# Performance work log

Hardware: AMD Instinct MI355X
Metric: run time of the kernel (lower is better)

The kernel has to match this reference:

```python
import jax, jax.numpy as jnp
from jax import lax
import numpy as np

NODE_COUNT = 4096
BATCH = 128
THRESHOLD = 1.0
DISSIPATION = 0.1
SPARSITY = 0.9
MAX_ITERS = 100


def setup_inputs() -> dict:
    key = jax.random.key(0)
    k_in, k_conn, k_mask, k_w, k_b = jax.random.split(key, 5)
    input_data = jax.random.normal(k_in, (BATCH, NODE_COUNT), dtype=jnp.float32)
    conn = jax.random.normal(k_conn, (NODE_COUNT, NODE_COUNT), dtype=jnp.float32)
    mask = (jax.random.uniform(k_mask, (NODE_COUNT, NODE_COUNT)) > SPARSITY).astype(jnp.float32)
    conn = conn * mask
    conn = conn / (jnp.abs(conn).sum(axis=1, keepdims=True) + 1e-6)
    # input_proj: Linear(node_count, node_count), torch default init scale
    bound = 1.0 / np.sqrt(NODE_COUNT)
    W = jax.random.uniform(k_w, (NODE_COUNT, NODE_COUNT), minval=-bound, maxval=bound, dtype=jnp.float32)
    b = jax.random.uniform(k_b, (NODE_COUNT,), minval=-bound, maxval=bound, dtype=jnp.float32)
    return {"input_data": input_data, "W": W, "b": b, "connections": conn}


def _avalanche(state, connections):
    """Batched avalanche scan with per-sample sticky early-exit (torch break)."""
    B = state.shape[0]
    done0 = jnp.zeros((B,), dtype=bool)
    total0 = jnp.zeros((B,), dtype=state.dtype)

    def step(carry, _):
        state, done, total = carry
        active = (state > THRESHOLD).astype(state.dtype)          # [B, N]
        n_active = active.sum(axis=1)                              # [B]
        new_done = done | (n_active == 0)                          # break condition
        total = total + jnp.where(new_done, 0.0, n_active)
        # propagated = connections @ active  (per sample)
        prop = jnp.einsum('ij,bj->bi', connections, active)        # [B, N]
        new_state = (state * (1.0 - DISSIPATION) + prop * (1.0 - active)) * (1.0 - active)
        state = jnp.where(new_done[:, None], state, new_state)
        return (state, new_done, total), None

    (state, done, total), _ = lax.scan(step, (state, done0, total0), None, length=MAX_ITERS)
    return state, total


def reference(input_data, W, b, connections):
    projected = input_data @ W.T + b                               # [B, N]
    output, sizes = _avalanche(projected, connections)
    max_size = sizes.max()
    return output, max_size
```

## Files before the change

### kernel.cpp

```cpp
#include <hip/hip_runtime.h>

#define N_NODES 4096
#define BATCH 128
#define SPLITK 8
#define GBN 32
#define GBK 64
#define KCHUNK (N_NODES / SPLITK)
#define NSTEP (KCHUNK / GBK)
#define GEMM_BLOCKS ((N_NODES / GBN) * SPLITK)
#define TRANS_BLOCKS 1024

typedef _Float16 f16x4 __attribute__((ext_vector_type(4)));
typedef _Float16 f16x8 __attribute__((ext_vector_type(8)));
typedef float f32x4 __attribute__((ext_vector_type(4)));
typedef unsigned int u32x4 __attribute__((ext_vector_type(4)));

__device__ __forceinline__ void dma16(const void* g, void* l) {
#if defined(__has_builtin) && __has_builtin(__builtin_amdgcn_global_load_lds)
  __builtin_amdgcn_global_load_lds((const __attribute__((address_space(1))) void*)g,
                                   (__attribute__((address_space(3))) void*)l, 16, 0, 0);
#else
  *(u32x4*)l = *(const u32x4*)g;
#endif
}

#if defined(__has_builtin)
#if __has_builtin(__builtin_amdgcn_cvt_f32_fp8) && __has_builtin(__builtin_amdgcn_cvt_pk_fp8_f32)
#define CONN_FP8 1
#endif
#endif
#ifndef CONN_FP8
#define CONN_FP8 0
#endif

#if CONN_FP8
#define CONN_ELEM_BYTES 1
#define CONN_SCALE (1.0f / 256.0f)
#else
#define CONN_ELEM_BYTES 2
#define CONN_SCALE 1.0f
#endif

__device__ __forceinline__ void conn_store4(void* out, size_t off, float4 v) {
#if CONN_FP8
  unsigned int p = __builtin_amdgcn_cvt_pk_fp8_f32(v.x * 256.0f, v.y * 256.0f, 0, false);
  p = (unsigned int)__builtin_amdgcn_cvt_pk_fp8_f32(v.z * 256.0f, v.w * 256.0f, (int)p, true);
  *(unsigned int*)((unsigned char*)out + off) = p;
#else
  const unsigned int ux = __float_as_uint(v.x), uy = __float_as_uint(v.y);
  const unsigned int uz = __float_as_uint(v.z), uw = __float_as_uint(v.w);
  ushort4 u;
  u.x = (unsigned short)((ux + 0x7FFFu + ((ux >> 16) & 1u)) >> 16);
  u.y = (unsigned short)((uy + 0x7FFFu + ((uy >> 16) & 1u)) >> 16);
  u.z = (unsigned short)((uz + 0x7FFFu + ((uz >> 16) & 1u)) >> 16);
  u.w = (unsigned short)((uw + 0x7FFFu + ((uw >> 16) & 1u)) >> 16);
  *(ushort4*)((unsigned short*)out + off) = u;
#endif
}

__device__ __forceinline__ float4 conn_load4(const void* cT, int j, int t) {
#if CONN_FP8
  const unsigned int c = *(const unsigned int*)((const unsigned char*)cT + ((size_t)j << 12) + t * 4);
  return make_float4(__builtin_amdgcn_cvt_f32_fp8(c, 0), __builtin_amdgcn_cvt_f32_fp8(c, 1),
                     __builtin_amdgcn_cvt_f32_fp8(c, 2), __builtin_amdgcn_cvt_f32_fp8(c, 3));
#else
  const ushort4 c = *(const ushort4*)((const unsigned short*)cT + ((size_t)j << 12) + t * 4);
  return make_float4(__uint_as_float((unsigned int)c.x << 16),
                     __uint_as_float((unsigned int)c.y << 16),
                     __uint_as_float((unsigned int)c.z << 16),
                     __uint_as_float((unsigned int)c.w << 16));
#endif
}

__global__ __launch_bounds__(256) void asplit_kernel(const float* __restrict__ in,
                                                     _Float16* __restrict__ Ah,
                                                     _Float16* __restrict__ Al,
                                                     unsigned int* __restrict__ maxslot) {
  if (blockIdx.x == 0 && threadIdx.x == 0) *maxslot = 0u;
  const size_t idx = ((size_t)blockIdx.x * 256 + threadIdx.x) * 4;
  const float4 v = *(const float4*)(in + idx);
  f16x4 hi, lo;
  const float x0 = v.x * 256.f, x1 = v.y * 256.f, x2 = v.z * 256.f, x3 = v.w * 256.f;
  hi[0] = (_Float16)x0; lo[0] = (_Float16)(x0 - (float)hi[0]);
  hi[1] = (_Float16)x1; lo[1] = (_Float16)(x1 - (float)hi[1]);
  hi[2] = (_Float16)x2; lo[2] = (_Float16)(x2 - (float)hi[2]);
  hi[3] = (_Float16)x3; lo[3] = (_Float16)(x3 - (float)hi[3]);
  *(f16x4*)(Ah + idx) = hi;
  *(f16x4*)(Al + idx) = lo;
}

struct GemmSmem {
  alignas(16) _Float16 Ah[2][128 * GBK];
  alignas(16) _Float16 Al[2][128 * GBK];
  alignas(16) float B[2][GBN * GBK];
};
struct TransSmem { float tile[4][64][65]; };
union PrepSmem { GemmSmem g; TransSmem t; };

__global__ __launch_bounds__(256, 2) void fused_prep_kernel(
    const _Float16* __restrict__ Ahp, const _Float16* __restrict__ Alp,
    const float* __restrict__ W, const float* __restrict__ conn,
    float* __restrict__ P, void* __restrict__ connT) {
  __shared__ PrepSmem sm;
  const int tid = threadIdx.x;
  const int bid = blockIdx.x;
  const int wave = tid >> 6, lane = tid & 63;

  if (bid < GEMM_BLOCKS) {
    const int wm = wave >> 1, wn = wave & 1;
    const int g = lane >> 4, lrow = lane & 15;
    const int n0 = (bid & 127) * GBN;
    const int kb = (bid >> 7) * KCHUNK;

    const char* AsrcBase = (const char*)((wave >> 1) ? Alp : Ahp);
    const int ac0 = (wave & 1) * 8;
    const int arow_l = lane >> 3;
    const int ainrow = (((lane & 7) << 4) ^ ((lane >> 3) << 4));
    const int brow_l = lane >> 4;
    const int binrow0 = (lane & 15) << 4;

    auto issue = [&](int buf, int t) {
      const size_t kbyteA = (size_t)(kb + t * GBK) * 2;
      const size_t kbyteB = (size_t)(kb + t * GBK) * 4;
      char* AldsB = (char*)((wave >> 1) ? sm.g.Al[buf] : sm.g.Ah[buf]);
#pragma unroll
      for (int i = 0; i < 8; ++i) {
        const int c = ac0 + i;
        const int row = 8 * c + arow_l;
        dma16(AsrcBase + (size_t)row * (N_NODES * 2) + kbyteA + ainrow,
              AldsB + c * 1024 + lane * 16);
      }
#pragma unroll
      for (int i = 0; i < 2; ++i) {
        const int c = wave * 2 + i;
        const int row = 4 * c + brow_l;
        dma16((const char*)W + (size_t)(n0 + row) * (N_NODES * 4) + kbyteB +
                  (binrow0 ^ ((row & 7) << 4)),
              (char*)sm.g.B[buf] + c * 1024 + lane * 16);
      }
    };

    f32x4 acc[4] = {};
    issue(0, 0);
    issue(1, 1);

#pragma unroll
    for (int t = 0; t < NSTEP; ++t) {
      const int cur = t & 1;
      if (t + 1 < NSTEP) asm volatile("s_waitcnt vmcnt(10)" ::: "memory");
      else               asm volatile("s_waitcnt vmcnt(0)" ::: "memory");
      __builtin_amdgcn_sched_barrier(0);
      __builtin_amdgcn_s_barrier();
      __builtin_amdgcn_sched_barrier(0);

#pragma unroll
      for (int kk = 0; kk < 2; ++kk) {
        const int br = wn * 16 + lrow;
        const char* bbase = (const char*)sm.g.B[cur] + br * 256;
        const int bm = (br & 7) << 4;
        const int cb = (kk * 32 + g * 8) * 4;
        const f32x4 b0 = *(const f32x4*)(bbase + ((cb) ^ bm));
        const f32x4 b1 = *(const f32x4*)(bbase + ((cb + 16) ^ bm));
        f16x8 bh, bl;
#pragma unroll
        for (int j = 0; j < 4; ++j) {
          const float x = b0[j] * 64.f;
          const _Float16 h = (_Float16)x;
          bh[j] = h; bl[j] = (_Float16)(x - (float)h);
          const float y = b1[j] * 64.f;
          const _Float16 h2 = (_Float16)y;
          bh[4 + j] = h2; bl[4 + j] = (_Float16)(y - (float)h2);
        }
#pragma unroll
        for (int fm = 0; fm < 4; ++fm) {
          const int ar = wm * 64 + fm * 16 + lrow;
          const int am = (ar & 7) << 4;
          const int ca = (kk * 32 + g * 8) * 2;
          const f16x8 ah = *(const f16x8*)((const char*)sm.g.Ah[cur] + ar * 128 + (ca ^ am));
          const f16x8 al = *(const f16x8*)((const char*)sm.g.Al[cur] + ar * 128 + (ca ^ am));
          acc[fm] = __builtin_amdgcn_mfma_f32_16x16x32_f16(ah, bh, acc[fm], 0, 0, 0);
          acc[fm] = __builtin_amdgcn_mfma_f32_16x16x32_f16(ah, bl, acc[fm], 0, 0, 0);
          acc[fm] = __builtin_amdgcn_mfma_f32_16x16x32_f16(al, bh, acc[fm], 0, 0, 0);
        }
      }

      __builtin_amdgcn_sched_barrier(0);
      __builtin_amdgcn_s_barrier();
      __builtin_amdgcn_sched_barrier(0);
      if (t + 2 < NSTEP) issue(cur, t + 2);
    }

    constexpr float INV = 1.0f / 16384.0f;
    float* Pb = P + (size_t)(bid >> 7) * BATCH * N_NODES;
    const int n = n0 + wn * 16 + lrow;
#pragma unroll
    for (int fm = 0; fm < 4; ++fm)
#pragma unroll
      for (int reg = 0; reg < 4; ++reg) {
        const int m = wm * 64 + fm * 16 + g * 4 + reg;
        Pb[(size_t)m * N_NODES + n] = acc[fm][reg] * INV;
      }
  } else {
    const int tile_id = (bid - GEMM_BLOCKS) * 4 + wave;
    const int bx = tile_id & 63, by = tile_id >> 6;
    float (*T)[65] = sm.t.tile[wave];
    const int lr = lane >> 4;
    const int lc = lane & 15;
#pragma unroll
    for (int i = 0; i < 16; ++i) {
      const int r = lr + 4 * i;
      const float4 v = *(const float4*)(conn + (size_t)(by * 64 + r) * N_NODES + bx * 64 + lc * 4);
      T[r][lc * 4 + 0] = v.x; T[r][lc * 4 + 1] = v.y;
      T[r][lc * 4 + 2] = v.z; T[r][lc * 4 + 3] = v.w;
    }
#pragma unroll
    for (int i = 0; i < 16; ++i) {
      const int orow = lr + 4 * i;
      float4 v;
      v.x = T[lc * 4 + 0][orow];
      v.y = T[lc * 4 + 1][orow];
      v.z = T[lc * 4 + 2][orow];
      v.w = T[lc * 4 + 3][orow];
      conn_store4(connT, (size_t)(bx * 64 + orow) * N_NODES + by * 64 + lc * 4, v);
    }
  }
}

__global__ __launch_bounds__(256) void proj_gemm_valu(const float* __restrict__ A,
                                                      const float* __restrict__ W,
                                                      float* __restrict__ P,
                                                      unsigned int* __restrict__ maxslot) {
  if (blockIdx.x == 0 && threadIdx.x == 0) *maxslot = 0u;
  __shared__ float As[16][132];
  __shared__ float Bs[16][68];
  const int tid = threadIdx.x;
  const int n0 = blockIdx.x * 64;
  const int tx = tid & 15, ty = tid >> 4;
  const int arow = tid >> 1, acol = (tid & 1) * 8;
  const int brow = tid >> 2, bcol = (tid & 3) * 4;
  float acc[2][4][4] = {};
  const float* Aptr = A + (size_t)arow * N_NODES + acol;
  const float* Wptr = W + (size_t)(n0 + brow) * N_NODES + bcol;
  for (int k0 = 0; k0 < N_NODES; k0 += 16) {
    const float4 a0 = *(const float4*)(Aptr + k0);
    const float4 a1 = *(const float4*)(Aptr + k0 + 4);
    const float4 bv = *(const float4*)(Wptr + k0);
    __syncthreads();
    As[acol + 0][arow] = a0.x; As[acol + 1][arow] = a0.y;
    As[acol + 2][arow] = a0.z; As[acol + 3][arow] = a0.w;
    As[acol + 4][arow] = a1.x; As[acol + 5][arow] = a1.y;
    As[acol + 6][arow] = a1.z; As[acol + 7][arow] = a1.w;
    Bs[bcol + 0][brow] = bv.x; Bs[bcol + 1][brow] = bv.y;
    Bs[bcol + 2][brow] = bv.z; Bs[bcol + 3][brow] = bv.w;
    __syncthreads();
#pragma unroll
    for (int kk = 0; kk < 16; ++kk) {
      const float4 av0 = *(const float4*)&As[kk][ty * 4];
      const float4 av1 = *(const float4*)&As[kk][64 + ty * 4];
      const float4 bv4 = *(const float4*)&Bs[kk][tx * 4];
      const float am[8] = {av0.x, av0.y, av0.z, av0.w, av1.x, av1.y, av1.z, av1.w};
      const float bn[4] = {bv4.x, bv4.y, bv4.z, bv4.w};
#pragma unroll
      for (int i2 = 0; i2 < 2; ++i2)
#pragma unroll
        for (int i = 0; i < 4; ++i)
#pragma unroll
          for (int j = 0; j < 4; ++j)
            acc[i2][i][j] += am[i2 * 4 + i] * bn[j];
    }
  }
#pragma unroll
  for (int i2 = 0; i2 < 2; ++i2)
#pragma unroll
    for (int i = 0; i < 4; ++i) {
      const int m = i2 * 64 + ty * 4 + i;
      *(float4*)(P + (size_t)m * N_NODES + n0 + tx * 4) =
          make_float4(acc[i2][i][0], acc[i2][i][1], acc[i2][i][2], acc[i2][i][3]);
    }
}

__global__ __launch_bounds__(256) void bias_inplace_kernel(float* __restrict__ P,
                                                           const float* __restrict__ bias) {
  const size_t base = ((size_t)blockIdx.x * 256 + threadIdx.x) * 4;
  const int n = (int)(base & (N_NODES - 1));
  float4 s = *(const float4*)(P + base);
  const float4 bv = *(const float4*)(bias + n);
  s.x += bv.x; s.y += bv.y; s.z += bv.z; s.w += bv.w;
  *(float4*)(P + base) = s;
}

template <int MODE, int NSPLIT>
__global__ __launch_bounds__(1024) void avalanche_kernel(const float* __restrict__ Pin,
                                                         const float* __restrict__ bias,
                                                         const void* __restrict__ connv,
                                                         float* __restrict__ out,
                                                         unsigned int* __restrict__ maxslot) {
  const int b = blockIdx.x;
  const int t = threadIdx.x;
  __shared__ unsigned long long mask[64];
  __shared__ int wincl[64];
  __shared__ int list[N_NODES];

  float4 s;
  if (MODE == 1) {
    const float4 bv = *(const float4*)(bias + t * 4);
    s = bv;
#pragma unroll
    for (int sp = 0; sp < NSPLIT; ++sp) {
      const float4 v = *(const float4*)(Pin + (size_t)sp * BATCH * N_NODES +
                                        (size_t)b * N_NODES + t * 4);
      s.x += v.x; s.y += v.y; s.z += v.z; s.w += v.w;
    }
  } else {
    s = *(const float4*)(Pin + (size_t)b * N_NODES + t * 4);
  }

  float total = 0.0f;

  for (int it = 0; it < 100; ++it) {
    const float v0 = s.x, v1 = s.y, v2 = s.z, v3 = s.w;
    unsigned int bits = 0;
    if (v0 > 1.0f) bits |= 1u;
    if (v1 > 1.0f) bits |= 2u;
    if (v2 > 1.0f) bits |= 4u;
    if (v3 > 1.0f) bits |= 8u;

    __syncthreads();
    if (t < 64) mask[t] = 0ULL;
    __syncthreads();
    if (bits) atomicOr(&mask[t >> 4], (unsigned long long)bits << ((t & 15) * 4));
    __syncthreads();

    if (t < 64) {
      int incl = __popcll(mask[t]);
#pragma unroll
      for (int d = 1; d < 64; d <<= 1) {
        const int y = __shfl_up(incl, d);
        if (t >= d) incl += y;
      }
      wincl[t] = incl;
    }
    __syncthreads();
    const int n = wincl[63];
    if (n == 0) break;
    total += (float)n;

    if (t < 64) {
      unsigned long long m = mask[t];
      int o = wincl[t] - __popcll(m);
      while (m) {
        list[o++] = (t << 6) + __builtin_ctzll(m);
        m &= m - 1;
      }
    }
    __syncthreads();

    float4 a0 = make_float4(0.f, 0.f, 0.f, 0.f), a1 = a0, a2 = a0, a3 = a0;
    if (MODE == 1) {
      int idx = 0;
      for (; idx + 8 <= n; idx += 8) {
        const float4 c0 = conn_load4(connv, list[idx + 0], t);
        const float4 c1 = conn_load4(connv, list[idx + 1], t);
        const float4 c2 = conn_load4(connv, list[idx + 2], t);
        const float4 c3 = conn_load4(connv, list[idx + 3], t);
        const float4 c4 = conn_load4(connv, list[idx + 4], t);
        const float4 c5 = conn_load4(connv, list[idx + 5], t);
        const float4 c6 = conn_load4(connv, list[idx + 6], t);
        const float4 c7 = conn_load4(connv, list[idx + 7], t);
        a0.x += c0.x; a0.y += c0.y; a0.z += c0.z; a0.w += c0.w;
        a1.x += c1.x; a1.y += c1.y; a1.z += c1.z; a1.w += c1.w;
        a2.x += c2.x; a2.y += c2.y; a2.z += c2.z; a2.w += c2.w;
        a3.x += c3.x; a3.y += c3.y; a3.z += c3.z; a3.w += c3.w;
        a0.x += c4.x; a0.y += c4.y; a0.z += c4.z; a0.w += c4.w;
        a1.x += c5.x; a1.y += c5.y; a1.z += c5.z; a1.w += c5.w;
        a2.x += c6.x; a2.y += c6.y; a2.z += c6.z; a2.w += c6.w;
        a3.x += c7.x; a3.y += c7.y; a3.z += c7.z; a3.w += c7.w;
      }
      for (; idx < n; ++idx) {
        const float4 c = conn_load4(connv, list[idx], t);
        a0.x += c.x; a0.y += c.y; a0.z += c.z; a0.w += c.w;
      }
    } else {
      const float* conn = (const float*)connv;
      for (int idx = 0; idx < n; ++idx) {
        const int j = list[idx];
        a0.x += conn[(size_t)(t * 4 + 0) * N_NODES + j];
        a0.y += conn[(size_t)(t * 4 + 1) * N_NODES + j];
        a0.z += conn[(size_t)(t * 4 + 2) * N_NODES + j];
        a0.w += conn[(size_t)(t * 4 + 3) * N_NODES + j];
      }
    }
    const float sc = (MODE == 1) ? CONN_SCALE : 1.0f;
    const float4 acc = make_float4(((a0.x + a1.x) + (a2.x + a3.x)) * sc,
                                   ((a0.y + a1.y) + (a2.y + a3.y)) * sc,
                                   ((a0.z + a1.z) + (a2.z + a3.z)) * sc,
                                   ((a0.w + a1.w) + (a2.w + a3.w)) * sc);

    s.x = (v0 > 1.0f) ? 0.0f : 0.9f * v0 + acc.x;
    s.y = (v1 > 1.0f) ? 0.0f : 0.9f * v1 + acc.y;
    s.z = (v2 > 1.0f) ? 0.0f : 0.9f * v2 + acc.z;
    s.w = (v3 > 1.0f) ? 0.0f : 0.9f * v3 + acc.w;
  }

  *(float4*)(out + (size_t)b * N_NODES + t * 4) = s;
  if (t == 0) atomicMax(maxslot, __float_as_uint(total));
}

extern "C" void kernel_launch(void* const* d_in, const int* in_sizes, int n_in,
                              void* d_out, int out_size, void* d_ws, size_t ws_size,
                              hipStream_t stream) {
  const float* input = (const float*)d_in[0];
  const float* W     = (const float*)d_in[1];
  const float* bias  = (const float*)d_in[2];
  const float* conn  = (const float*)d_in[3];
  float* out = (float*)d_out;

  const size_t aplane_bytes = (size_t)BATCH * N_NODES * 2;
  const size_t connT_bytes  = (size_t)N_NODES * N_NODES * CONN_ELEM_BYTES;
  const size_t part_bytes   = (size_t)SPLITK * BATCH * N_NODES * sizeof(float);
  unsigned int* maxslot = (unsigned int*)(out + (size_t)BATCH * N_NODES);

  if (ws_size >= 2 * aplane_bytes + connT_bytes + part_bytes) {
    _Float16* Ah = (_Float16*)d_ws;
    _Float16* Al = (_Float16*)((char*)d_ws + aplane_bytes);
    void* connT  = (char*)d_ws + 2 * aplane_bytes;
    float* part  = (float*)((char*)d_ws + 2 * aplane_bytes + connT_bytes);
    asplit_kernel<<<BATCH * N_NODES / 1024, 256, 0, stream>>>(input, Ah, Al, maxslot);
    fused_prep_kernel<<<GEMM_BLOCKS + TRANS_BLOCKS, 256, 0, stream>>>(Ah, Al, W, conn, part,
                                                                      connT);
    avalanche_kernel<1, SPLITK><<<BATCH, 1024, 0, stream>>>(part, bias, connT, out, maxslot);
  } else {
    proj_gemm_valu<<<dim3(N_NODES / 64, 1), 256, 0, stream>>>(input, W, out, maxslot);
    bias_inplace_kernel<<<BATCH * N_NODES / 1024, 256, 0, stream>>>(out, bias);
    avalanche_kernel<0, 1><<<BATCH, 1024, 0, stream>>>(out, nullptr, conn, out, maxslot);
  }
}
```

Measured before the change: 70.17 us.

## Enlarge GEMM tile to 128x128 with interleaved hi/lo A layout

Restructures the projection GEMM so each block computes a 128x128 output tile, up from 128x32. It reads W once per block and splits it into hi/lo halves once per fragment, then reuses those fragments across four M-fragments, which cuts redundant W traffic and conversion work. The input split now writes hi and lo halves interleaved into a single buffer, so one DMA stream feeds both. Split-K doubles to 16, which doubles the partial-sum buffer the avalanche kernel must reduce, and the 4x4 accumulator array raises register pressure.

```diff
diff --git a/kernel.cpp b/kernel.cpp
--- a/kernel.cpp
+++ b/kernel.cpp
@@ -2,9 +2,9 @@
 
 #define N_NODES 4096
 #define BATCH 128
-#define SPLITK 8
-#define GBN 32
-#define GBK 64
+#define SPLITK 16
+#define GBN 128
+#define GBK 32
 #define KCHUNK (N_NODES / SPLITK)
 #define NSTEP (KCHUNK / GBK)
 #define GEMM_BLOCKS ((N_NODES / GBN) * SPLITK)
@@ -73,11 +73,12 @@
 }
 
 __global__ __launch_bounds__(256) void asplit_kernel(const float* __restrict__ in,
-                                                     _Float16* __restrict__ Ah,
-                                                     _Float16* __restrict__ Al,
+                                                     _Float16* __restrict__ As,
                                                      unsigned int* __restrict__ maxslot) {
   if (blockIdx.x == 0 && threadIdx.x == 0) *maxslot = 0u;
   const size_t idx = ((size_t)blockIdx.x * 256 + threadIdx.x) * 4;
+  const int m = (int)(idx >> 12);
+  const int k = (int)(idx & (N_NODES - 1));
   const float4 v = *(const float4*)(in + idx);
   f16x4 hi, lo;
   const float x0 = v.x * 256.f, x1 = v.y * 256.f, x2 = v.z * 256.f, x3 = v.w * 256.f;
@@ -85,22 +86,21 @@
   hi[1] = (_Float16)x1; lo[1] = (_Float16)(x1 - (float)hi[1]);
   hi[2] = (_Float16)x2; lo[2] = (_Float16)(x2 - (float)hi[2]);
   hi[3] = (_Float16)x3; lo[3] = (_Float16)(x3 - (float)hi[3]);
-  *(f16x4*)(Ah + idx) = hi;
-  *(f16x4*)(Al + idx) = lo;
+  const size_t base = (size_t)m * 8192 + (size_t)(k >> 5) * 64 + (k & 31);
+  *(f16x4*)(As + base) = hi;
+  *(f16x4*)(As + base + 32) = lo;
 }
 
 struct GemmSmem {
-  alignas(16) _Float16 Ah[2][128 * GBK];
-  alignas(16) _Float16 Al[2][128 * GBK];
-  alignas(16) float B[2][GBN * GBK];
+  alignas(16) _Float16 A[2][128 * 64];
+  alignas(16) float B[2][128 * 32];
 };
 struct TransSmem { float tile[4][64][65]; };
 union PrepSmem { GemmSmem g; TransSmem t; };
 
 __global__ __launch_bounds__(256, 2) void fused_prep_kernel(
-    const _Float16* __restrict__ Ahp, const _Float16* __restrict__ Alp,
-    const float* __restrict__ W, const float* __restrict__ conn,
-    float* __restrict__ P, void* __restrict__ connT) {
+    const _Float16* __restrict__ As, const float* __restrict__ W,
+    const float* __restrict__ conn, float* __restrict__ P, void* __restrict__ connT) {
   __shared__ PrepSmem sm;
   const int tid = threadIdx.x;
   const int bid = blockIdx.x;
@@ -109,80 +109,78 @@
   if (bid < GEMM_BLOCKS) {
     const int wm = wave >> 1, wn = wave & 1;
     const int g = lane >> 4, lrow = lane & 15;
-    const int n0 = (bid & 127) * GBN;
-    const int kb = (bid >> 7) * KCHUNK;
-
-    const char* AsrcBase = (const char*)((wave >> 1) ? Alp : Ahp);
-    const int ac0 = (wave & 1) * 8;
-    const int arow_l = lane >> 3;
-    const int ainrow = (((lane & 7) << 4) ^ ((lane >> 3) << 4));
-    const int brow_l = lane >> 4;
-    const int binrow0 = (lane & 15) << 4;
+    const int n0 = (bid & 31) * GBN;
+    const int kb = (bid >> 5) * KCHUNK;
+    const int crow = lane >> 3;
+    const int q = lane & 7;
 
     auto issue = [&](int buf, int t) {
-      const size_t kbyteA = (size_t)(kb + t * GBK) * 2;
-      const size_t kbyteB = (size_t)(kb + t * GBK) * 4;
-      char* AldsB = (char*)((wave >> 1) ? sm.g.Al[buf] : sm.g.Ah[buf]);
-#pragma unroll
-      for (int i = 0; i < 8; ++i) {
-        const int c = ac0 + i;
-        const int row = 8 * c + arow_l;
-        dma16(AsrcBase + (size_t)row * (N_NODES * 2) + kbyteA + ainrow,
-              AldsB + c * 1024 + lane * 16);
-      }
-#pragma unroll
-      for (int i = 0; i < 2; ++i) {
-        const int c = wave * 2 + i;
-        const int row = 4 * c + brow_l;
-        dma16((const char*)W + (size_t)(n0 + row) * (N_NODES * 4) + kbyteB +
-                  (binrow0 ^ ((row & 7) << 4)),
+      const size_t abyte = (size_t)((kb >> 5) + t) * 128;
+      const size_t bbyte = (size_t)(kb + t * GBK) * 4;
+#pragma unroll
+      for (int i = 0; i < 4; ++i) {
+        const int c = wave * 4 + i;
+        const int row = c * 8 + crow;
+        dma16((const char*)As + (size_t)row * 16384 + abyte + ((q ^ crow) << 4),
+              (char*)sm.g.A[buf] + c * 1024 + lane * 16);
+      }
+#pragma unroll
+      for (int i = 0; i < 4; ++i) {
+        const int c = wave * 4 + i;
+        const int row = c * 8 + crow;
+        dma16((const char*)W + (size_t)(n0 + row) * 16384 + bbyte + ((q ^ crow) << 4),
               (char*)sm.g.B[buf] + c * 1024 + lane * 16);
       }
     };
 
-    f32x4 acc[4] = {};
+    f32x4 acc[4][4] = {};
     issue(0, 0);
     issue(1, 1);
 
 #pragma unroll
     for (int t = 0; t < NSTEP; ++t) {
       const int cur = t & 1;
-      if (t + 1 < NSTEP) asm volatile("s_waitcnt vmcnt(10)" ::: "memory");
+      if (t + 1 < NSTEP) asm volatile("s_waitcnt vmcnt(8)" ::: "memory");
       else               asm volatile("s_waitcnt vmcnt(0)" ::: "memory");
       __builtin_amdgcn_sched_barrier(0);
       __builtin_amdgcn_s_barrier();
       __builtin_amdgcn_sched_barrier(0);
 
-#pragma unroll
-      for (int kk = 0; kk < 2; ++kk) {
-        const int br = wn * 16 + lrow;
-        const char* bbase = (const char*)sm.g.B[cur] + br * 256;
-        const int bm = (br & 7) << 4;
-        const int cb = (kk * 32 + g * 8) * 4;
-        const f32x4 b0 = *(const f32x4*)(bbase + ((cb) ^ bm));
-        const f32x4 b1 = *(const f32x4*)(bbase + ((cb + 16) ^ bm));
-        f16x8 bh, bl;
+      f16x8 ah[4], al[4];
+#pragma unroll
+      for (int fm = 0; fm < 4; ++fm) {
+        const int mr = wm * 64 + fm * 16 + lrow;
+        const char* ab = (const char*)sm.g.A[cur] + mr * 128;
+        const int s = (mr & 7) << 4;
+        ah[fm] = *(const f16x8*)(ab + ((g << 4) ^ s));
+        al[fm] = *(const f16x8*)(ab + (((4 + g) << 4) ^ s));
+      }
+      f16x8 bh[4], bl[4];
+#pragma unroll
+      for (int fn = 0; fn < 4; ++fn) {
+        const int nr = wn * 64 + fn * 16 + lrow;
+        const char* bb = (const char*)sm.g.B[cur] + nr * 128;
+        const int s = (nr & 7) << 4;
+        const f32x4 b0 = *(const f32x4*)(bb + (((2 * g) << 4) ^ s));
+        const f32x4 b1 = *(const f32x4*)(bb + (((2 * g + 1) << 4) ^ s));
 #pragma unroll
         for (int j = 0; j < 4; ++j) {
           const float x = b0[j] * 64.f;
           const _Float16 h = (_Float16)x;
-          bh[j] = h; bl[j] = (_Float16)(x - (float)h);
+          bh[fn][j] = h; bl[fn][j] = (_Float16)(x - (float)h);
           const float y = b1[j] * 64.f;
           const _Float16 h2 = (_Float16)y;
-          bh[4 + j] = h2; bl[4 + j] = (_Float16)(y - (float)h2);
+          bh[fn][4 + j] = h2; bl[fn][4 + j] = (_Float16)(y - (float)h2);
         }
-#pragma unroll
-        for (int fm = 0; fm < 4; ++fm) {
-          const int ar = wm * 64 + fm * 16 + lrow;
-          const int am = (ar & 7) << 4;
-          const int ca = (kk * 32 + g * 8) * 2;
-          const f16x8 ah = *(const f16x8*)((const char*)sm.g.Ah[cur] + ar * 128 + (ca ^ am));
-          const f16x8 al = *(const f16x8*)((const char*)sm.g.Al[cur] + ar * 128 + (ca ^ am));
-          acc[fm] = __builtin_amdgcn_mfma_f32_16x16x32_f16(ah, bh, acc[fm], 0, 0, 0);
-          acc[fm] = __builtin_amdgcn_mfma_f32_16x16x32_f16(ah, bl, acc[fm], 0, 0, 0);
-          acc[fm] = __builtin_amdgcn_mfma_f32_16x16x32_f16(al, bh, acc[fm], 0, 0, 0);
+      }
+#pragma unroll
+      for (int fm = 0; fm < 4; ++fm)
+#pragma unroll
+        for (int fn = 0; fn < 4; ++fn) {
+          acc[fm][fn] = __builtin_amdgcn_mfma_f32_16x16x32_f16(ah[fm], bh[fn], acc[fm][fn], 0, 0, 0);
+          acc[fm][fn] = __builtin_amdgcn_mfma_f32_16x16x32_f16(ah[fm], bl[fn], acc[fm][fn], 0, 0, 0);
+          acc[fm][fn] = __builtin_amdgcn_mfma_f32_16x16x32_f16(al[fm], bh[fn], acc[fm][fn], 0, 0, 0);
         }
-      }
 
       __builtin_amdgcn_sched_barrier(0);
       __builtin_amdgcn_s_barrier();
@@ -191,14 +189,17 @@
     }
 
     constexpr float INV = 1.0f / 16384.0f;
-    float* Pb = P + (size_t)(bid >> 7) * BATCH * N_NODES;
-    const int n = n0 + wn * 16 + lrow;
+    float* Pb = P + (size_t)(bid >> 5) * BATCH * N_NODES;
 #pragma unroll
     for (int fm = 0; fm < 4; ++fm)
 #pragma unroll
-      for (int reg = 0; reg < 4; ++reg) {
-        const int m = wm * 64 + fm * 16 + g * 4 + reg;
-        Pb[(size_t)m * N_NODES + n] = acc[fm][reg] * INV;
+      for (int fn = 0; fn < 4; ++fn) {
+        const int n = n0 + wn * 64 + fn * 16 + lrow;
+#pragma unroll
+        for (int reg = 0; reg < 4; ++reg) {
+          const int m = wm * 64 + fm * 16 + g * 4 + reg;
+          Pb[(size_t)m * N_NODES + n] = acc[fm][fn][reg] * INV;
+        }
       }
   } else {
     const int tile_id = (bid - GEMM_BLOCKS) * 4 + wave;
@@ -231,8 +232,8 @@
                                                       float* __restrict__ P,
                                                       unsigned int* __restrict__ maxslot) {
   if (blockIdx.x == 0 && threadIdx.x == 0) *maxslot = 0u;
-  __shared__ float As[16][132];
-  __shared__ float Bs[16][68];
+  __shared__ float Asb[16][132];
+  __shared__ float Bsb[16][68];
   const int tid = threadIdx.x;
   const int n0 = blockIdx.x * 64;
   const int tx = tid & 15, ty = tid >> 4;
@@ -246,18 +247,18 @@
     const float4 a1 = *(const float4*)(Aptr + k0 + 4);
     const float4 bv = *(const float4*)(Wptr + k0);
     __syncthreads();
-    As[acol + 0][arow] = a0.x; As[acol + 1][arow] = a0.y;
-    As[acol + 2][arow] = a0.z; As[acol + 3][arow] = a0.w;
-    As[acol + 4][arow] = a1.x; As[acol + 5][arow] = a1.y;
-    As[acol + 6][arow] = a1.z; As[acol + 7][arow] = a1.w;
-    Bs[bcol + 0][brow] = bv.x; Bs[bcol + 1][brow] = bv.y;
-    Bs[bcol + 2][brow] = bv.z; Bs[bcol + 3][brow] = bv.w;
+    Asb[acol + 0][arow] = a0.x; Asb[acol + 1][arow] = a0.y;
+    Asb[acol + 2][arow] = a0.z; Asb[acol + 3][arow] = a0.w;
+    Asb[acol + 4][arow] = a1.x; Asb[acol + 5][arow] = a1.y;
+    Asb[acol + 6][arow] = a1.z; Asb[acol + 7][arow] = a1.w;
+    Bsb[bcol + 0][brow] = bv.x; Bsb[bcol + 1][brow] = bv.y;
+    Bsb[bcol + 2][brow] = bv.z; Bsb[bcol + 3][brow] = bv.w;
     __syncthreads();
 #pragma unroll
     for (int kk = 0; kk < 16; ++kk) {
-      const float4 av0 = *(const float4*)&As[kk][ty * 4];
-      const float4 av1 = *(const float4*)&As[kk][64 + ty * 4];
-      const float4 bv4 = *(const float4*)&Bs[kk][tx * 4];
+      const float4 av0 = *(const float4*)&Asb[kk][ty * 4];
+      const float4 av1 = *(const float4*)&Asb[kk][64 + ty * 4];
+      const float4 bv4 = *(const float4*)&Bsb[kk][tx * 4];
       const float am[8] = {av0.x, av0.y, av0.z, av0.w, av1.x, av1.y, av1.z, av1.w};
       const float bn[4] = {bv4.x, bv4.y, bv4.z, bv4.w};
 #pragma unroll
@@ -415,19 +416,17 @@
   const float* conn  = (const float*)d_in[3];
   float* out = (float*)d_out;
 
-  const size_t aplane_bytes = (size_t)BATCH * N_NODES * 2;
+  const size_t aplane_bytes = (size_t)BATCH * N_NODES * 4;
   const size_t connT_bytes  = (size_t)N_NODES * N_NODES * CONN_ELEM_BYTES;
   const size_t part_bytes   = (size_t)SPLITK * BATCH * N_NODES * sizeof(float);
   unsigned int* maxslot = (unsigned int*)(out + (size_t)BATCH * N_NODES);
 
-  if (ws_size >= 2 * aplane_bytes + connT_bytes + part_bytes) {
-    _Float16* Ah = (_Float16*)d_ws;
-    _Float16* Al = (_Float16*)((char*)d_ws + aplane_bytes);
-    void* connT  = (char*)d_ws + 2 * aplane_bytes;
-    float* part  = (float*)((char*)d_ws + 2 * aplane_bytes + connT_bytes);
-    asplit_kernel<<<BATCH * N_NODES / 1024, 256, 0, stream>>>(input, Ah, Al, maxslot);
-    fused_prep_kernel<<<GEMM_BLOCKS + TRANS_BLOCKS, 256, 0, stream>>>(Ah, Al, W, conn, part,
-                                                                      connT);
+  if (ws_size >= aplane_bytes + connT_bytes + part_bytes) {
+    _Float16* As = (_Float16*)d_ws;
+    void* connT  = (char*)d_ws + aplane_bytes;
+    float* part  = (float*)((char*)d_ws + aplane_bytes + connT_bytes);
+    asplit_kernel<<<BATCH * N_NODES / 1024, 256, 0, stream>>>(input, As, maxslot);
+    fused_prep_kernel<<<GEMM_BLOCKS + TRANS_BLOCKS, 256, 0, stream>>>(As, W, conn, part, connT);
     avalanche_kernel<1, SPLITK><<<BATCH, 1024, 0, stream>>>(part, bias, connT, out, maxslot);
   } else {
     proj_gemm_valu<<<dim3(N_NODES / 64, 1), 256, 0, stream>>>(input, W, out, maxslot);
```

Result: no change. 69.50 us (-0.9%).
